# Kernel optimization log

Measured on AMD Instinct MI355X. Metric: run time of the kernel, lower is better.

Reference implementation:

```python
import jax, jax.numpy as jnp
import numpy as np
from jax import lax

UPDATE_RATE = 0.5
DT = 1.0

IDENTITY = jnp.array([[0.0, 0.0, 0.0], [0.0, 1.0, 0.0], [0.0, 0.0, 0.0]], jnp.float32)
LAPLACIAN = jnp.array([[1.0, 2.0, 1.0], [2.0, -12.0, 2.0], [1.0, 2.0, 1.0]], jnp.float32)
SOBEL_H = jnp.array([[-1.0, -1.0, -1.0], [0.0, 0.0, 0.0], [1.0, 1.0, 1.0]], jnp.float32)
SOBEL_W = jnp.array([[-1.0, 0.0, 1.0], [-1.0, 0.0, 1.0], [-1.0, 0.0, 1.0]], jnp.float32)
MOORE = jnp.array([[1.0, 1.0, 1.0], [1.0, 0.0, 1.0], [1.0, 1.0, 1.0]], jnp.float32)


def setup_inputs() -> dict:
    key = jax.random.key(0)
    k0, k1, k2, k3 = jax.random.split(key, 4)
    B, C, H, W = 16, 8, 512, 512
    F = 5  # number_filters
    HID = 32  # number_hidden
    grid = jax.random.uniform(k0, (B, C, H, W), dtype=jnp.float32)
    noise = jax.random.uniform(k1, (B, C, H, W), dtype=jnp.float32)  # drives update mask
    filters = jnp.stack([IDENTITY, LAPLACIAN, SOBEL_H, SOBEL_W, MOORE])  # [F,3,3]
    # conv_0 weight [hidden, C*F, 1, 1]; conv_1 weight [C, hidden, 1, 1]
    w0 = jax.random.normal(k2, (HID, C * F, 1, 1), dtype=jnp.float32) * 0.1
    w1 = jax.random.normal(k3, (C, HID, 1, 1), dtype=jnp.float32) * 0.1
    return {"grid": grid, "noise": noise, "filters": filters, "w0": w0, "w1": w1}


def perceive(grid, filters):
    # Depthwise: each of C channels convolved with each of F 3x3 stencils -> [B, C*F, H, W]
    B, C, H, W = grid.shape
    F = filters.shape[0]
    gp = jnp.pad(grid, ((0, 0), (0, 0), (1, 1), (1, 1)), mode="wrap")  # circular pad
    kernel = jnp.tile(filters[None, :, :, :], (C, 1, 1, 1)).reshape(C * F, 1, 3, 3)
    return lax.conv_general_dilated(
        gp, kernel, window_strides=(1, 1), padding="VALID",
        feature_group_count=C,
        dimension_numbers=("NCHW", "OIHW", "NCHW"),
    )


def reference(grid, noise, filters, w0, w1):
    mask = (noise < UPDATE_RATE).astype(grid.dtype)
    percep = perceive(grid, filters)                      # [B, C*F, H, W]
    h = jnp.einsum("bfhw,of->bohw", percep, w0[:, :, 0, 0])  # 1x1 conv_0
    y = jnp.einsum("bohw,co->bchw", h, w1[:, :, 0, 0])        # 1x1 conv_1
    new_grid = grid + DT * y * mask
    return jnp.clip(new_grid, 0.0, 1.0)  # hard_clamp squash
```

## Files before the change

### kernel.cpp

```cpp
#include <hip/hip_runtime.h>


#define B_ 16
#define C_ 8
#define H_ 512
#define W_ 512
#define HID_ 32
#define F_ 5

#define TH 16
#define TW 64

__global__ void nca_prep(const float* __restrict__ filters,
                         const float* __restrict__ w0,
                         const float* __restrict__ w1,
                         float* __restrict__ K)
{
    int idx = blockIdx.x * blockDim.x + threadIdx.x;
    if (idx >= C_ * C_ * 9) return;
    int k  = idx % 9;
    int t  = idx / 9;
    int cp = t % C_;
    int c  = t / C_;
    float acc = 0.f;
    #pragma unroll
    for (int f = 0; f < F_; ++f) {
        float we = 0.f;
        for (int o = 0; o < HID_; ++o)
            we += w1[c * HID_ + o] * w0[o * (C_ * F_) + cp * F_ + f];
        acc += we * filters[f * 9 + k];
    }
    K[idx] = acc;
}

__global__ __launch_bounds__(256) void nca_main(
    const float* __restrict__ grid,
    const float* __restrict__ noise,
    const float* __restrict__ K,
    float* __restrict__ out)
{
    __shared__ float lds[C_][TH + 2][TW + 2];

    const int b  = blockIdx.z;
    const int h0 = blockIdx.y * TH;
    const int w0 = blockIdx.x * TW;
    const int tid = threadIdx.x;

    const int PER_CH = (TH + 2) * (TW + 2);
    const int TOTAL  = C_ * PER_CH;
    for (int i = tid; i < TOTAL; i += 256) {
        int c   = i / PER_CH;
        int rem = i - c * PER_CH;
        int r   = rem / (TW + 2);
        int col = rem - r * (TW + 2);
        int gh  = (h0 + r - 1) & (H_ - 1);
        int gw  = (w0 + col - 1) & (W_ - 1);
        (&lds[0][0][0])[i] = grid[(((b << 3) + c) << 18) + (gh << 9) + gw];
    }
    __syncthreads();

    const int lw  = tid & 63;
    const int lh0 = (tid >> 6) << 2;

    float acc[C_][4];
    #pragma unroll
    for (int c = 0; c < C_; ++c)
        #pragma unroll
        for (int p = 0; p < 4; ++p) acc[c][p] = 0.f;

    for (int cp = 0; cp < C_; ++cp) {
        float v[6][3];
        #pragma unroll
        for (int r = 0; r < 6; ++r)
            #pragma unroll
            for (int cc = 0; cc < 3; ++cc)
                v[r][cc] = lds[cp][lh0 + r][lw + cc];

        #pragma unroll
        for (int c = 0; c < C_; ++c) {
            #pragma unroll
            for (int kh = 0; kh < 3; ++kh) {
                #pragma unroll
                for (int kw = 0; kw < 3; ++kw) {
                    const float kv = K[(c * C_ + cp) * 9 + kh * 3 + kw];
                    #pragma unroll
                    for (int p = 0; p < 4; ++p)
                        acc[c][p] += kv * v[p + kh][kw];
                }
            }
        }
    }

    #pragma unroll
    for (int c = 0; c < C_; ++c) {
        #pragma unroll
        for (int p = 0; p < 4; ++p) {
            const int h  = h0 + lh0 + p;
            const int gi = (((b << 3) + c) << 18) + (h << 9) + (w0 + lw);
            const float g = lds[c][lh0 + p + 1][lw + 1];
            const float m = (noise[gi] < 0.5f) ? 1.0f : 0.0f;
            float nv = g + acc[c][p] * m;
            nv = fminf(fmaxf(nv, 0.0f), 1.0f);
            out[gi] = nv;
        }
    }
}

extern "C" void kernel_launch(void* const* d_in, const int* in_sizes, int n_in,
                              void* d_out, int out_size, void* d_ws, size_t ws_size,
                              hipStream_t stream)
{
    const float* grid    = (const float*)d_in[0];
    const float* noise   = (const float*)d_in[1];
    const float* filters = (const float*)d_in[2];
    const float* w0      = (const float*)d_in[3];
    const float* w1      = (const float*)d_in[4];
    float* out = (float*)d_out;
    float* K   = (float*)d_ws;

    nca_prep<<<1, 576, 0, stream>>>(filters, w0, w1, K);

    dim3 g(W_ / TW, H_ / TH, B_);
    nca_main<<<g, 256, 0, stream>>>(grid, noise, K, out);
}
```

Measured before the change: 113.3 us.

## Stage channels in two LDS halves and compute 2x2 output blocks

Shared memory is halved by loading the halo tile in two groups of four channels with a sync between them. Occupancy is raised with a launch-bounds hint of five blocks per SIMD. Each thread now computes a 2x2 output patch instead of a 4x1 column, reading LDS with float2 loads and writing noise/out with float2 accesses. The trade-offs are an extra barrier and sequential load/compute phases, plus register pressure from keeping centre values for the first group.

```diff
diff --git a/kernel.cpp b/kernel.cpp
--- a/kernel.cpp
+++ b/kernel.cpp
@@ -10,6 +10,9 @@
 
 #define TH 16
 #define TW 64
+#define GC 4
+#define PER_CH ((TH + 2) * (TW + 2))
+#define GROUP_ELEMS (GC * PER_CH)
 
 __global__ void nca_prep(const float* __restrict__ filters,
                          const float* __restrict__ w0,
@@ -33,34 +36,22 @@
     K[idx] = acc;
 }
 
-__global__ __launch_bounds__(256) void nca_main(
+__global__ __launch_bounds__(256, 5) void nca_main(
     const float* __restrict__ grid,
     const float* __restrict__ noise,
     const float* __restrict__ K,
     float* __restrict__ out)
 {
-    __shared__ float lds[C_][TH + 2][TW + 2];
+    __shared__ float lds[GC][TH + 2][TW + 2];
 
-    const int b  = blockIdx.z;
-    const int h0 = blockIdx.y * TH;
-    const int w0 = blockIdx.x * TW;
+    const int b   = blockIdx.z;
+    const int h0  = blockIdx.y * TH;
+    const int w0c = blockIdx.x * TW;
     const int tid = threadIdx.x;
-
-    const int PER_CH = (TH + 2) * (TW + 2);
-    const int TOTAL  = C_ * PER_CH;
-    for (int i = tid; i < TOTAL; i += 256) {
-        int c   = i / PER_CH;
-        int rem = i - c * PER_CH;
-        int r   = rem / (TW + 2);
-        int col = rem - r * (TW + 2);
-        int gh  = (h0 + r - 1) & (H_ - 1);
-        int gw  = (w0 + col - 1) & (W_ - 1);
-        (&lds[0][0][0])[i] = grid[(((b << 3) + c) << 18) + (gh << 9) + gw];
-    }
-    __syncthreads();
-
-    const int lw  = tid & 63;
-    const int lh0 = (tid >> 6) << 2;
+    const int tx  = tid & 31;
+    const int ty  = tid >> 5;
+    const int lw2 = tx << 1;
+    const int R0  = ty << 1;
 
     float acc[C_][4];
     #pragma unroll
@@ -68,40 +59,84 @@
         #pragma unroll
         for (int p = 0; p < 4; ++p) acc[c][p] = 0.f;
 
-    for (int cp = 0; cp < C_; ++cp) {
-        float v[6][3];
-        #pragma unroll
-        for (int r = 0; r < 6; ++r)
-            #pragma unroll
-            for (int cc = 0; cc < 3; ++cc)
-                v[r][cc] = lds[cp][lh0 + r][lw + cc];
+    float cen[GC][4];
+
+    const int c_init   = tid / PER_CH;
+    const int rem_init = tid - c_init * PER_CH;
+    const int r_init   = rem_init / (TW + 2);
+    const int col_init = rem_init - r_init * (TW + 2);
+
+    float* lflat = &lds[0][0][0];
+
+    #pragma unroll
+    for (int g = 0; g < 2; ++g) {
+        {
+            int c = c_init, r = r_init, col = col_init;
+            for (int i = tid; i < GROUP_ELEMS; i += 256) {
+                const int gh = (h0 + r - 1) & (H_ - 1);
+                const int gw = (w0c + col - 1) & (W_ - 1);
+                lflat[i] = grid[(((b << 3) + (g << 2) + c) << 18) + (gh << 9) + gw];
+                col += 58; r += 3;
+                if (col >= TW + 2) { col -= TW + 2; ++r; }
+                if (r >= TH + 2)   { r -= TH + 2; ++c; }
+            }
+        }
+        __syncthreads();
 
         #pragma unroll
-        for (int c = 0; c < C_; ++c) {
+        for (int cp = 0; cp < GC; ++cp) {
+            float w[4][4];
             #pragma unroll
-            for (int kh = 0; kh < 3; ++kh) {
+            for (int r = 0; r < 4; ++r) {
+                const float2* p = reinterpret_cast<const float2*>(&lds[cp][R0 + r][lw2]);
+                float2 a = p[0];
+                float2 bb = p[1];
+                w[r][0] = a.x; w[r][1] = a.y; w[r][2] = bb.x; w[r][3] = bb.y;
+            }
+            if (g == 0) {
+                cen[cp][0] = w[1][1]; cen[cp][1] = w[1][2];
+                cen[cp][2] = w[2][1]; cen[cp][3] = w[2][2];
+            }
+            const int gcp = (g << 2) + cp;
+            #pragma unroll
+            for (int c = 0; c < C_; ++c) {
+                const float* __restrict__ kk = K + (c * C_ + gcp) * 9;
                 #pragma unroll
-                for (int kw = 0; kw < 3; ++kw) {
-                    const float kv = K[(c * C_ + cp) * 9 + kh * 3 + kw];
+                for (int kh = 0; kh < 3; ++kh) {
                     #pragma unroll
-                    for (int p = 0; p < 4; ++p)
-                        acc[c][p] += kv * v[p + kh][kw];
+                    for (int kw = 0; kw < 3; ++kw) {
+                        const float kv = kk[kh * 3 + kw];
+                        acc[c][0] += kv * w[0 + kh][0 + kw];
+                        acc[c][1] += kv * w[0 + kh][1 + kw];
+                        acc[c][2] += kv * w[1 + kh][0 + kw];
+                        acc[c][3] += kv * w[1 + kh][1 + kw];
+                    }
                 }
             }
         }
+        if (g == 0) __syncthreads();
     }
 
     #pragma unroll
     for (int c = 0; c < C_; ++c) {
         #pragma unroll
-        for (int p = 0; p < 4; ++p) {
-            const int h  = h0 + lh0 + p;
-            const int gi = (((b << 3) + c) << 18) + (h << 9) + (w0 + lw);
-            const float g = lds[c][lh0 + p + 1][lw + 1];
-            const float m = (noise[gi] < 0.5f) ? 1.0f : 0.0f;
-            float nv = g + acc[c][p] * m;
-            nv = fminf(fmaxf(nv, 0.0f), 1.0f);
-            out[gi] = nv;
+        for (int pr = 0; pr < 2; ++pr) {
+            const int h  = h0 + R0 + pr;
+            const int gi = (((b << 3) + c) << 18) + (h << 9) + (w0c + lw2);
+            const float2 nz = *reinterpret_cast<const float2*>(&noise[gi]);
+            float g0, g1;
+            if (c < GC) {
+                g0 = cen[c][pr * 2 + 0];
+                g1 = cen[c][pr * 2 + 1];
+            } else {
+                g0 = lds[c - GC][R0 + 1 + pr][lw2 + 1];
+                g1 = lds[c - GC][R0 + 1 + pr][lw2 + 2];
+            }
+            float o0 = (nz.x < 0.5f) ? (g0 + acc[c][pr * 2 + 0]) : g0;
+            float o1 = (nz.y < 0.5f) ? (g1 + acc[c][pr * 2 + 1]) : g1;
+            o0 = fminf(fmaxf(o0, 0.0f), 1.0f);
+            o1 = fminf(fmaxf(o1, 0.0f), 1.0f);
+            *reinterpret_cast<float2*>(&out[gi]) = make_float2(o0, o1);
         }
     }
 }
```

After: 193.7 us. 70.9% more time.
